# Optimization experiments

Measured on AMD Instinct MI355X. Metric: run time of the kernel, lower is better.

## Reference

```python
import jax, jax.numpy as jnp
import numpy as np

N = 100000
E = 3200000
F_IN = 512
H = 16
C = 40


def gcn_conv(x, edge_index, W, b, num_nodes):
    """PyG GCNConv: y = D^{-1/2} (A + I) D^{-1/2} (x @ W) + b.
    edge_index: [2, E] int, row=source, col=target; self-loops added here."""
    # transform first (small hidden dim keeps message traffic low)
    h = x @ W  # [N, out]
    loops = jnp.arange(num_nodes, dtype=edge_index.dtype)
    row = jnp.concatenate([edge_index[0], loops])
    col = jnp.concatenate([edge_index[1], loops])
    deg = jax.ops.segment_sum(jnp.ones_like(col, dtype=h.dtype), col,
                              num_segments=num_nodes)  # in-degree incl. self-loop
    dinv = jnp.where(deg > 0, jax.lax.rsqrt(deg), 0.0)
    norm = dinv[row] * dinv[col]  # [E+N]
    msgs = h[row] * norm[:, None]  # gather + scale, [E+N, out]
    out = jax.ops.segment_sum(msgs, col, num_segments=num_nodes)  # scatter-add
    return out + b


def setup_inputs() -> dict:
    key = jax.random.key(0)
    k1, k2, k3, k4, k5, k6 = jax.random.split(key, 6)
    x = jax.random.normal(k1, (N, F_IN), dtype=jnp.float32)
    edge_index = jax.random.randint(k2, (2, E), 0, N, dtype=jnp.int64)
    s1 = 1.0 / np.sqrt(F_IN)
    s2 = 1.0 / np.sqrt(H)
    W1 = jax.random.uniform(k3, (F_IN, H), jnp.float32, -s1, s1)
    b1 = jnp.zeros((H,), jnp.float32)
    W2 = jax.random.uniform(k4, (H, C), jnp.float32, -s2, s2)
    b2 = jnp.zeros((C,), jnp.float32)
    return {"x": x, "edge_index": edge_index, "W1": W1, "b1": b1,
            "W2": W2, "b2": b2}


def reference(x, edge_index, W1, b1, W2, b2):
    h = gcn_conv(x, edge_index, W1, b1, N)
    h = jax.nn.relu(h)
    # F.dropout(training=self.training): inference mode -> identity
    h = gcn_conv(h, edge_index, W2, b2, N)
    return jax.nn.log_softmax(h, axis=1)
```

## Files before the change

### kernel.cpp

```cpp
#include <hip/hip_runtime.h>

#define NN 100000
#define EE 3200000
#define FIN 512
#define HH 16
#define CC 40

#define SHIFT 9
#define BNODES 512
#define NB 196
#define CAP 20480
#define CH 4096
#define TC ((EE + CH - 1) / CH)

__device__ __forceinline__ float bf2f(unsigned short u) {
    return __uint_as_float(((unsigned)u) << 16);
}
__device__ __forceinline__ unsigned short f2bf(float f) {
    unsigned b = __float_as_uint(f);
    return (unsigned short)((b + 0x7FFF + ((b >> 16) & 1)) >> 16);
}

__global__ void k_detect(const int* __restrict__ ei, int* __restrict__ flag) {
    __shared__ int nz;
    int t = threadIdx.x;
    if (t == 0) nz = 0;
    __syncthreads();
    if (ei[2 * t + 1] != 0) atomicAdd(&nz, 1);
    __syncthreads();
    if (t == 0) flag[0] = (nz == 0) ? 1 : 0;
}

__global__ void k_bin(const int* __restrict__ ei, const int* __restrict__ flag,
                      int* __restrict__ head, unsigned* __restrict__ pairs) {
    __shared__ int h[NB];
    __shared__ int gbase[NB];
    __shared__ int lhead[NB];
    int t = threadIdx.x;
    int e0 = blockIdx.x * CH, e1 = min(EE, e0 + CH);
    int is64 = flag[0];
    for (int i = t; i < NB; i += 256) { h[i] = 0; lhead[i] = 0; }
    __syncthreads();
    for (int e = e0 + t; e < e1; e += 256) {
        int dst = is64 ? ei[2 * (EE + e)] : ei[EE + e];
        atomicAdd(&h[dst >> SHIFT], 1);
    }
    __syncthreads();
    for (int i = t; i < NB; i += 256)
        gbase[i] = h[i] ? atomicAdd(&head[i], h[i]) : 0;
    __syncthreads();
    for (int e = e0 + t; e < e1; e += 256) {
        int src = is64 ? ei[2 * e] : ei[e];
        int dst = is64 ? ei[2 * (EE + e)] : ei[EE + e];
        int b = dst >> SHIFT;
        int p = gbase[b] + atomicAdd(&lhead[b], 1);
        pairs[(size_t)b * CAP + p] = ((unsigned)(dst & (BNODES - 1)) << 17) | (unsigned)src;
    }
}

__global__ void k_build(const unsigned* __restrict__ pairs, const int* __restrict__ head,
                        int* __restrict__ ptr, int* __restrict__ pend,
                        float* __restrict__ dinv, int* __restrict__ srcs) {
    __shared__ int h[BNODES];
    __shared__ int lex[BNODES];
    __shared__ int ws[4];
    int b = blockIdx.x, t = threadIdx.x, lane = t & 63, wid = t >> 6;
    int node0 = b << SHIFT;
    int p0 = b * CAP;
    int cnt = head[b];
    for (int i = t; i < BNODES; i += 256) h[i] = 0;
    __syncthreads();
    for (int p = t; p < cnt; p += 256) atomicAdd(&h[pairs[p0 + p] >> 17], 1);
    __syncthreads();
    int a0 = h[2 * t], a1 = h[2 * t + 1];
    int s = a0 + a1;
    int v = s;
#pragma unroll
    for (int off = 1; off < 64; off <<= 1) {
        int u = __shfl_up(v, off);
        if (lane >= off) v += u;
    }
    if (lane == 63) ws[wid] = v;
    __syncthreads();
    int add = 0;
    for (int w = 0; w < wid; ++w) add += ws[w];
    int incl = v + add;
    int e0 = incl - s;
    lex[2 * t] = e0;
    lex[2 * t + 1] = e0 + a0;
    __syncthreads();
    for (int i = t; i < BNODES; i += 256) {
        int n = node0 + i;
        if (n < NN) {
            int st = p0 + lex[i];
            ptr[n] = st;
            pend[n] = st + h[i];
            dinv[n] = rsqrtf((float)(h[i] + 1));
        }
    }
    __syncthreads();
    for (int p = t; p < cnt; p += 256) {
        unsigned w = pairs[p0 + p];
        int pos = p0 + atomicAdd(&lex[w >> 17], 1);
        srcs[pos] = (int)(w & 0x1FFFF);
    }
}

__global__ void __launch_bounds__(256) k_gemm1(const float* __restrict__ x,
                                               const float* __restrict__ W1,
                                               const float* __restrict__ dinv,
                                               unsigned short* __restrict__ g1) {
    __shared__ float w1s[FIN * HH];
    int t = threadIdx.x;
    for (int i = t; i < FIN * HH; i += 256) w1s[i] = W1[i];
    __syncthreads();
    int gt = blockIdx.x * 256 + t;
    int node = gt >> 2, q = gt & 3;
    if (node >= NN) return;
    const float4* xr = reinterpret_cast<const float4*>(x + (size_t)node * FIN + q * 128);
    float acc[HH];
#pragma unroll
    for (int f = 0; f < HH; ++f) acc[f] = 0.f;
#pragma unroll 4
    for (int kq = 0; kq < 32; ++kq) {
        float4 xv = xr[kq];
        const float* wr = w1s + (q * 128 + kq * 4) * HH;
#pragma unroll
        for (int f = 0; f < HH; ++f) acc[f] = fmaf(xv.x, wr[f], acc[f]);
#pragma unroll
        for (int f = 0; f < HH; ++f) acc[f] = fmaf(xv.y, wr[HH + f], acc[f]);
#pragma unroll
        for (int f = 0; f < HH; ++f) acc[f] = fmaf(xv.z, wr[2 * HH + f], acc[f]);
#pragma unroll
        for (int f = 0; f < HH; ++f) acc[f] = fmaf(xv.w, wr[3 * HH + f], acc[f]);
    }
#pragma unroll
    for (int f = 0; f < HH; ++f) {
        acc[f] += __shfl_xor(acc[f], 1);
        acc[f] += __shfl_xor(acc[f], 2);
    }
    float di = dinv[node];
    ushort4 o;
    o.x = f2bf(acc[4 * q + 0] * di);
    o.y = f2bf(acc[4 * q + 1] * di);
    o.z = f2bf(acc[4 * q + 2] * di);
    o.w = f2bf(acc[4 * q + 3] * di);
    reinterpret_cast<ushort4*>(g1)[node * 4 + q] = o;
}

__global__ void k_agg1(const unsigned short* __restrict__ g1, const int* __restrict__ ptr,
                       const int* __restrict__ pend, const int* __restrict__ srcs,
                       const float* __restrict__ dinv, const float* __restrict__ b1,
                       unsigned short* __restrict__ g2h) {
    int gt = blockIdx.x * blockDim.x + threadIdx.x;
    int node = gt >> 2, q = gt & 3;
    if (node >= NN) return;
    const ushort4* G = reinterpret_cast<const ushort4*>(g1);
    ushort4 sv = G[node * 4 + q];
    float ax = bf2f(sv.x), ay = bf2f(sv.y), az = bf2f(sv.z), aw = bf2f(sv.w);
    float bx = 0.f, by = 0.f, bz = 0.f, bw = 0.f;
    float cx = 0.f, cy = 0.f, cz = 0.f, cw = 0.f;
    float dx = 0.f, dy = 0.f, dz = 0.f, dw = 0.f;
    int e = ptr[node], e1 = pend[node];
    for (; e + 3 < e1; e += 4) {
        int s0 = srcs[e], s1 = srcs[e + 1], s2 = srcs[e + 2], s3 = srcs[e + 3];
        ushort4 v0 = G[s0 * 4 + q];
        ushort4 v1 = G[s1 * 4 + q];
        ushort4 v2 = G[s2 * 4 + q];
        ushort4 v3 = G[s3 * 4 + q];
        ax += bf2f(v0.x); ay += bf2f(v0.y); az += bf2f(v0.z); aw += bf2f(v0.w);
        bx += bf2f(v1.x); by += bf2f(v1.y); bz += bf2f(v1.z); bw += bf2f(v1.w);
        cx += bf2f(v2.x); cy += bf2f(v2.y); cz += bf2f(v2.z); cw += bf2f(v2.w);
        dx += bf2f(v3.x); dy += bf2f(v3.y); dz += bf2f(v3.z); dw += bf2f(v3.w);
    }
    for (; e < e1; ++e) {
        ushort4 v = G[srcs[e] * 4 + q];
        ax += bf2f(v.x); ay += bf2f(v.y); az += bf2f(v.z); aw += bf2f(v.w);
    }
    ax += bx + cx + dx;
    ay += by + cy + dy;
    az += bz + cz + dz;
    aw += bw + cw + dw;
    float di = dinv[node];
    const float4 bb = reinterpret_cast<const float4*>(b1)[q];
    ushort4 r;
    r.x = f2bf(fmaxf(fmaf(di, ax, bb.x), 0.f) * di);
    r.y = f2bf(fmaxf(fmaf(di, ay, bb.y), 0.f) * di);
    r.z = f2bf(fmaxf(fmaf(di, az, bb.z), 0.f) * di);
    r.w = f2bf(fmaxf(fmaf(di, aw, bb.w), 0.f) * di);
    reinterpret_cast<ushort4*>(g2h)[node * 4 + q] = r;
}

__global__ void k_agg2(const unsigned short* __restrict__ g2h, const int* __restrict__ ptr,
                       const int* __restrict__ pend, const int* __restrict__ srcs,
                       float* __restrict__ sarr) {
    int gt = blockIdx.x * blockDim.x + threadIdx.x;
    int node = gt >> 2, q = gt & 3;
    if (node >= NN) return;
    const ushort4* G = reinterpret_cast<const ushort4*>(g2h);
    ushort4 sv = G[node * 4 + q];
    float ax = bf2f(sv.x), ay = bf2f(sv.y), az = bf2f(sv.z), aw = bf2f(sv.w);
    float bx = 0.f, by = 0.f, bz = 0.f, bw = 0.f;
    float cx = 0.f, cy = 0.f, cz = 0.f, cw = 0.f;
    float dx = 0.f, dy = 0.f, dz = 0.f, dw = 0.f;
    int e = ptr[node], e1 = pend[node];
    for (; e + 3 < e1; e += 4) {
        int s0 = srcs[e], s1 = srcs[e + 1], s2 = srcs[e + 2], s3 = srcs[e + 3];
        ushort4 v0 = G[s0 * 4 + q];
        ushort4 v1 = G[s1 * 4 + q];
        ushort4 v2 = G[s2 * 4 + q];
        ushort4 v3 = G[s3 * 4 + q];
        ax += bf2f(v0.x); ay += bf2f(v0.y); az += bf2f(v0.z); aw += bf2f(v0.w);
        bx += bf2f(v1.x); by += bf2f(v1.y); bz += bf2f(v1.z); bw += bf2f(v1.w);
        cx += bf2f(v2.x); cy += bf2f(v2.y); cz += bf2f(v2.z); cw += bf2f(v2.w);
        dx += bf2f(v3.x); dy += bf2f(v3.y); dz += bf2f(v3.z); dw += bf2f(v3.w);
    }
    for (; e < e1; ++e) {
        ushort4 v = G[srcs[e] * 4 + q];
        ax += bf2f(v.x); ay += bf2f(v.y); az += bf2f(v.z); aw += bf2f(v.w);
    }
    ax += bx + cx + dx;
    ay += by + cy + dy;
    az += bz + cz + dz;
    aw += bw + cw + dw;
    reinterpret_cast<float4*>(sarr)[node * 4 + q] = make_float4(ax, ay, az, aw);
}

__global__ void k_out(const float* __restrict__ sarr, const float* __restrict__ dinv,
                      const float* __restrict__ W2, const float* __restrict__ b2,
                      float* __restrict__ out) {
    int i = blockIdx.x * blockDim.x + threadIdx.x;
    if (i >= NN) return;
    float s[HH];
    {
        const float4* sp = reinterpret_cast<const float4*>(sarr + (size_t)i * HH);
#pragma unroll
        for (int qk = 0; qk < HH / 4; ++qk) {
            float4 v = sp[qk];
            s[4 * qk] = v.x; s[4 * qk + 1] = v.y; s[4 * qk + 2] = v.z; s[4 * qk + 3] = v.w;
        }
    }
    float di = dinv[i];
    float y[CC];
#pragma unroll
    for (int c = 0; c < CC; ++c) y[c] = 0.f;
#pragma unroll
    for (int f = 0; f < HH; ++f) {
        float sf = s[f];
        const float* w2r = W2 + f * CC;
#pragma unroll
        for (int c = 0; c < CC; ++c) y[c] = fmaf(sf, w2r[c], y[c]);
    }
    float m = -3.0e38f;
#pragma unroll
    for (int c = 0; c < CC; ++c) {
        y[c] = fmaf(di, y[c], b2[c]);
        m = fmaxf(m, y[c]);
    }
    float ssum = 0.f;
#pragma unroll
    for (int c = 0; c < CC; ++c) ssum += expf(y[c] - m);
    float l = logf(ssum) + m;
    float4* o = reinterpret_cast<float4*>(out + (size_t)i * CC);
#pragma unroll
    for (int qk = 0; qk < CC / 4; ++qk)
        o[qk] = make_float4(y[4 * qk] - l, y[4 * qk + 1] - l,
                            y[4 * qk + 2] - l, y[4 * qk + 3] - l);
}

extern "C" void kernel_launch(void* const* d_in, const int* in_sizes, int n_in,
                              void* d_out, int out_size, void* d_ws, size_t ws_size,
                              hipStream_t stream) {
    const float* x  = (const float*)d_in[0];
    const int*   ei = (const int*)d_in[1];
    const float* W1 = (const float*)d_in[2];
    const float* b1 = (const float*)d_in[3];
    const float* W2 = (const float*)d_in[4];
    const float* b2 = (const float*)d_in[5];
    float* out = (float*)d_out;

    char* w = (char*)d_ws;
    auto alloc = [&](size_t bytes) {
        char* p = w;
        w += (bytes + 255) & ~(size_t)255;
        return p;
    };
    int*            flag  = (int*)alloc(256);
    int*            head  = (int*)alloc((size_t)NB * 4);
    int*            ptr   = (int*)alloc((size_t)NN * 4);
    int*            pend  = (int*)alloc((size_t)NN * 4);
    float*          dinv  = (float*)alloc((size_t)NN * 4);
    unsigned*       pairs = (unsigned*)alloc((size_t)NB * CAP * 4);
    int*            srcs  = (int*)alloc((size_t)NB * CAP * 4);
    unsigned short* g1    = (unsigned short*)alloc((size_t)NN * HH * 2);
    unsigned short* g2h   = (unsigned short*)alloc((size_t)NN * HH * 2);
    float*          sarr  = (float*)alloc((size_t)NN * HH * 4);

    hipMemsetAsync(head, 0, (size_t)NB * sizeof(int), stream);
    k_detect<<<1, 256, 0, stream>>>(ei, flag);
    k_bin<<<TC, 256, 0, stream>>>(ei, flag, head, pairs);
    k_build<<<NB, 256, 0, stream>>>(pairs, head, ptr, pend, dinv, srcs);
    int nt = NN * 4;
    k_gemm1<<<(nt + 255) / 256, 256, 0, stream>>>(x, W1, dinv, g1);
    k_agg1<<<(nt + 255) / 256, 256, 0, stream>>>(g1, ptr, pend, srcs, dinv, b1, g2h);
    k_agg2<<<(nt + 255) / 256, 256, 0, stream>>>(g2h, ptr, pend, srcs, sarr);
    k_out<<<(NN + 255) / 256, 256, 0, stream>>>(sarr, dinv, W2, b2, out);
}
```

Before: 522.6 us.

## Fuse CSR build with GEMM1, agg2 with output, stage edges in LDS

```diff
diff --git a/kernel.cpp b/kernel.cpp
--- a/kernel.cpp
+++ b/kernel.cpp
@@ -10,8 +10,9 @@
 #define BNODES 512
 #define NB 196
 #define CAP 20480
-#define CH 4096
+#define CH 2048
 #define TC ((EE + CH - 1) / CH)
+#define GB ((NN * 4 + 255) / 256)
 
 __device__ __forceinline__ float bf2f(unsigned short u) {
     return __uint_as_float(((unsigned)u) << 16);
@@ -21,130 +22,143 @@
     return (unsigned short)((b + 0x7FFF + ((b >> 16) & 1)) >> 16);
 }
 
-__global__ void k_detect(const int* __restrict__ ei, int* __restrict__ flag) {
-    __shared__ int nz;
-    int t = threadIdx.x;
-    if (t == 0) nz = 0;
-    __syncthreads();
-    if (ei[2 * t + 1] != 0) atomicAdd(&nz, 1);
-    __syncthreads();
-    if (t == 0) flag[0] = (nz == 0) ? 1 : 0;
-}
-
-__global__ void k_bin(const int* __restrict__ ei, const int* __restrict__ flag,
-                      int* __restrict__ head, unsigned* __restrict__ pairs) {
+__global__ void k_bin(const int* __restrict__ ei, int* __restrict__ head,
+                      unsigned* __restrict__ pairs) {
     __shared__ int h[NB];
     __shared__ int gbase[NB];
     __shared__ int lhead[NB];
+    __shared__ unsigned esrc[CH];
+    __shared__ unsigned edst[CH];
+    __shared__ int is64_s;
     int t = threadIdx.x;
-    int e0 = blockIdx.x * CH, e1 = min(EE, e0 + CH);
-    int is64 = flag[0];
+    if (t < 64) {
+        int nz = (ei[2 * t + 1] != 0) ? 1 : 0;
+        unsigned long long m = __ballot(nz);
+        if (t == 0) is64_s = (m == 0ULL) ? 1 : 0;
+    }
     for (int i = t; i < NB; i += 256) { h[i] = 0; lhead[i] = 0; }
     __syncthreads();
+    int is64 = is64_s;
+    int e0 = blockIdx.x * CH, e1 = min(EE, e0 + CH);
     for (int e = e0 + t; e < e1; e += 256) {
+        int src = is64 ? ei[2 * e] : ei[e];
         int dst = is64 ? ei[2 * (EE + e)] : ei[EE + e];
+        esrc[e - e0] = (unsigned)src;
+        edst[e - e0] = (unsigned)dst;
         atomicAdd(&h[dst >> SHIFT], 1);
     }
     __syncthreads();
     for (int i = t; i < NB; i += 256)
         gbase[i] = h[i] ? atomicAdd(&head[i], h[i]) : 0;
     __syncthreads();
-    for (int e = e0 + t; e < e1; e += 256) {
-        int src = is64 ? ei[2 * e] : ei[e];
-        int dst = is64 ? ei[2 * (EE + e)] : ei[EE + e];
-        int b = dst >> SHIFT;
+    int n = e1 - e0;
+    for (int j = t; j < n; j += 256) {
+        unsigned src = esrc[j];
+        unsigned dst = edst[j];
+        int b = (int)(dst >> SHIFT);
         int p = gbase[b] + atomicAdd(&lhead[b], 1);
-        pairs[(size_t)b * CAP + p] = ((unsigned)(dst & (BNODES - 1)) << 17) | (unsigned)src;
-    }
-}
-
-__global__ void k_build(const unsigned* __restrict__ pairs, const int* __restrict__ head,
-                        int* __restrict__ ptr, int* __restrict__ pend,
-                        float* __restrict__ dinv, int* __restrict__ srcs) {
-    __shared__ int h[BNODES];
-    __shared__ int lex[BNODES];
-    __shared__ int ws[4];
-    int b = blockIdx.x, t = threadIdx.x, lane = t & 63, wid = t >> 6;
-    int node0 = b << SHIFT;
-    int p0 = b * CAP;
-    int cnt = head[b];
-    for (int i = t; i < BNODES; i += 256) h[i] = 0;
-    __syncthreads();
-    for (int p = t; p < cnt; p += 256) atomicAdd(&h[pairs[p0 + p] >> 17], 1);
-    __syncthreads();
-    int a0 = h[2 * t], a1 = h[2 * t + 1];
-    int s = a0 + a1;
-    int v = s;
-#pragma unroll
-    for (int off = 1; off < 64; off <<= 1) {
-        int u = __shfl_up(v, off);
-        if (lane >= off) v += u;
-    }
-    if (lane == 63) ws[wid] = v;
-    __syncthreads();
-    int add = 0;
-    for (int w = 0; w < wid; ++w) add += ws[w];
-    int incl = v + add;
-    int e0 = incl - s;
-    lex[2 * t] = e0;
-    lex[2 * t + 1] = e0 + a0;
-    __syncthreads();
-    for (int i = t; i < BNODES; i += 256) {
-        int n = node0 + i;
-        if (n < NN) {
-            int st = p0 + lex[i];
-            ptr[n] = st;
-            pend[n] = st + h[i];
-            dinv[n] = rsqrtf((float)(h[i] + 1));
-        }
-    }
-    __syncthreads();
-    for (int p = t; p < cnt; p += 256) {
-        unsigned w = pairs[p0 + p];
-        int pos = p0 + atomicAdd(&lex[w >> 17], 1);
-        srcs[pos] = (int)(w & 0x1FFFF);
-    }
-}
-
-__global__ void __launch_bounds__(256) k_gemm1(const float* __restrict__ x,
-                                               const float* __restrict__ W1,
-                                               const float* __restrict__ dinv,
-                                               unsigned short* __restrict__ g1) {
+        pairs[(size_t)b * CAP + p] = ((dst & (BNODES - 1)) << 17) | src;
+    }
+}
+
+__global__ void __launch_bounds__(256) k_buildgemm(
+        const unsigned* __restrict__ pairs, const int* __restrict__ head,
+        int* __restrict__ ptr, int* __restrict__ pend,
+        float* __restrict__ dinv, int* __restrict__ srcs,
+        const float* __restrict__ x, const float* __restrict__ W1,
+        float* __restrict__ g1f) {
     __shared__ float w1s[FIN * HH];
     int t = threadIdx.x;
-    for (int i = t; i < FIN * HH; i += 256) w1s[i] = W1[i];
-    __syncthreads();
-    int gt = blockIdx.x * 256 + t;
+    if (blockIdx.x < NB) {
+        int* h   = (int*)w1s;
+        int* lex = (int*)w1s + BNODES;
+        int* ws  = (int*)w1s + 2 * BNODES;
+        int b = blockIdx.x, lane = t & 63, wid = t >> 6;
+        int node0 = b << SHIFT;
+        int p0 = b * CAP;
+        int cnt = head[b];
+        for (int i = t; i < BNODES; i += 256) h[i] = 0;
+        __syncthreads();
+        for (int p = t; p < cnt; p += 256) atomicAdd(&h[pairs[p0 + p] >> 17], 1);
+        __syncthreads();
+        int a0 = h[2 * t], a1 = h[2 * t + 1];
+        int s = a0 + a1;
+        int v = s;
+#pragma unroll
+        for (int off = 1; off < 64; off <<= 1) {
+            int u = __shfl_up(v, off);
+            if (lane >= off) v += u;
+        }
+        if (lane == 63) ws[wid] = v;
+        __syncthreads();
+        int add = 0;
+        for (int w = 0; w < wid; ++w) add += ws[w];
+        int incl = v + add;
+        int e0 = incl - s;
+        lex[2 * t] = e0;
+        lex[2 * t + 1] = e0 + a0;
+        __syncthreads();
+        for (int i = t; i < BNODES; i += 256) {
+            int n = node0 + i;
+            if (n < NN) {
+                int st = p0 + lex[i];
+                ptr[n] = st;
+                pend[n] = st + h[i];
+                dinv[n] = rsqrtf((float)(h[i] + 1));
+            }
+        }
+        __syncthreads();
+        for (int p = t; p < cnt; p += 256) {
+            unsigned w = pairs[p0 + p];
+            int pos = p0 + atomicAdd(&lex[w >> 17], 1);
+            srcs[pos] = (int)(w & 0x1FFFF);
+        }
+    } else {
+        for (int i = t; i < FIN * HH; i += 256) w1s[i] = W1[i];
+        __syncthreads();
+        int gt = (blockIdx.x - NB) * 256 + t;
+        int node = gt >> 2, q = gt & 3;
+        if (node >= NN) return;
+        const float4* xr = reinterpret_cast<const float4*>(x + (size_t)node * FIN + q * 128);
+        float acc[HH];
+#pragma unroll
+        for (int f = 0; f < HH; ++f) acc[f] = 0.f;
+#pragma unroll 4
+        for (int kq = 0; kq < 32; ++kq) {
+            float4 xv = xr[kq];
+            const float* wr = w1s + (q * 128 + kq * 4) * HH;
+#pragma unroll
+            for (int f = 0; f < HH; ++f) acc[f] = fmaf(xv.x, wr[f], acc[f]);
+#pragma unroll
+            for (int f = 0; f < HH; ++f) acc[f] = fmaf(xv.y, wr[HH + f], acc[f]);
+#pragma unroll
+            for (int f = 0; f < HH; ++f) acc[f] = fmaf(xv.z, wr[2 * HH + f], acc[f]);
+#pragma unroll
+            for (int f = 0; f < HH; ++f) acc[f] = fmaf(xv.w, wr[3 * HH + f], acc[f]);
+        }
+#pragma unroll
+        for (int f = 0; f < HH; ++f) {
+            acc[f] += __shfl_xor(acc[f], 1);
+            acc[f] += __shfl_xor(acc[f], 2);
+        }
+        float4 o = make_float4(acc[4 * q + 0], acc[4 * q + 1],
+                               acc[4 * q + 2], acc[4 * q + 3]);
+        reinterpret_cast<float4*>(g1f)[node * 4 + q] = o;
+    }
+}
+
+__global__ void k_scale(const float* __restrict__ g1f, const float* __restrict__ dinv,
+                        unsigned short* __restrict__ g1) {
+    int gt = blockIdx.x * 256 + threadIdx.x;
     int node = gt >> 2, q = gt & 3;
     if (node >= NN) return;
-    const float4* xr = reinterpret_cast<const float4*>(x + (size_t)node * FIN + q * 128);
-    float acc[HH];
-#pragma unroll
-    for (int f = 0; f < HH; ++f) acc[f] = 0.f;
-#pragma unroll 4
-    for (int kq = 0; kq < 32; ++kq) {
-        float4 xv = xr[kq];
-        const float* wr = w1s + (q * 128 + kq * 4) * HH;
-#pragma unroll
-        for (int f = 0; f < HH; ++f) acc[f] = fmaf(xv.x, wr[f], acc[f]);
-#pragma unroll
-        for (int f = 0; f < HH; ++f) acc[f] = fmaf(xv.y, wr[HH + f], acc[f]);
-#pragma unroll
-        for (int f = 0; f < HH; ++f) acc[f] = fmaf(xv.z, wr[2 * HH + f], acc[f]);
-#pragma unroll
-        for (int f = 0; f < HH; ++f) acc[f] = fmaf(xv.w, wr[3 * HH + f], acc[f]);
-    }
-#pragma unroll
-    for (int f = 0; f < HH; ++f) {
-        acc[f] += __shfl_xor(acc[f], 1);
-        acc[f] += __shfl_xor(acc[f], 2);
-    }
     float di = dinv[node];
+    float4 v = reinterpret_cast<const float4*>(g1f)[node * 4 + q];
     ushort4 o;
-    o.x = f2bf(acc[4 * q + 0] * di);
-    o.y = f2bf(acc[4 * q + 1] * di);
-    o.z = f2bf(acc[4 * q + 2] * di);
-    o.w = f2bf(acc[4 * q + 3] * di);
+    o.x = f2bf(v.x * di);
+    o.y = f2bf(v.y * di);
+    o.z = f2bf(v.z * di);
+    o.w = f2bf(v.w * di);
     reinterpret_cast<ushort4*>(g1)[node * 4 + q] = o;
 }
 
@@ -191,10 +205,18 @@
     reinterpret_cast<ushort4*>(g2h)[node * 4 + q] = r;
 }
 
-__global__ void k_agg2(const unsigned short* __restrict__ g2h, const int* __restrict__ ptr,
-                       const int* __restrict__ pend, const int* __restrict__ srcs,
-                       float* __restrict__ sarr) {
-    int gt = blockIdx.x * blockDim.x + threadIdx.x;
+__global__ void __launch_bounds__(256) k_agg2out(
+        const unsigned short* __restrict__ g2h, const int* __restrict__ ptr,
+        const int* __restrict__ pend, const int* __restrict__ srcs,
+        const float* __restrict__ dinv, const float* __restrict__ W2,
+        const float* __restrict__ b2, float* __restrict__ out) {
+    __shared__ float w2s[HH * 41];
+    __shared__ float b2s[CC];
+    int t = threadIdx.x;
+    for (int i = t; i < HH * CC; i += 256) w2s[(i / CC) * 41 + (i % CC)] = W2[i];
+    if (t < CC) b2s[t] = b2[t];
+    __syncthreads();
+    int gt = blockIdx.x * blockDim.x + t;
     int node = gt >> 2, q = gt & 3;
     if (node >= NN) return;
     const ushort4* G = reinterpret_cast<const ushort4*>(g2h);
@@ -223,49 +245,38 @@
     ay += by + cy + dy;
     az += bz + cz + dz;
     aw += bw + cw + dw;
-    reinterpret_cast<float4*>(sarr)[node * 4 + q] = make_float4(ax, ay, az, aw);
-}
-
-__global__ void k_out(const float* __restrict__ sarr, const float* __restrict__ dinv,
-                      const float* __restrict__ W2, const float* __restrict__ b2,
-                      float* __restrict__ out) {
-    int i = blockIdx.x * blockDim.x + threadIdx.x;
-    if (i >= NN) return;
-    float s[HH];
-    {
-        const float4* sp = reinterpret_cast<const float4*>(sarr + (size_t)i * HH);
-#pragma unroll
-        for (int qk = 0; qk < HH / 4; ++qk) {
-            float4 v = sp[qk];
-            s[4 * qk] = v.x; s[4 * qk + 1] = v.y; s[4 * qk + 2] = v.z; s[4 * qk + 3] = v.w;
-        }
-    }
-    float di = dinv[i];
+    const float* w0 = w2s + (4 * q + 0) * 41;
+    const float* w1 = w2s + (4 * q + 1) * 41;
+    const float* w2r = w2s + (4 * q + 2) * 41;
+    const float* w3 = w2s + (4 * q + 3) * 41;
     float y[CC];
 #pragma unroll
-    for (int c = 0; c < CC; ++c) y[c] = 0.f;
-#pragma unroll
-    for (int f = 0; f < HH; ++f) {
-        float sf = s[f];
-        const float* w2r = W2 + f * CC;
-#pragma unroll
-        for (int c = 0; c < CC; ++c) y[c] = fmaf(sf, w2r[c], y[c]);
-    }
+    for (int c = 0; c < CC; ++c)
+        y[c] = fmaf(ax, w0[c], fmaf(ay, w1[c], fmaf(az, w2r[c], aw * w3[c])));
+#pragma unroll
+    for (int c = 0; c < CC; ++c) {
+        y[c] += __shfl_xor(y[c], 1);
+        y[c] += __shfl_xor(y[c], 2);
+    }
+    float di = dinv[node];
     float m = -3.0e38f;
 #pragma unroll
     for (int c = 0; c < CC; ++c) {
-        y[c] = fmaf(di, y[c], b2[c]);
+        y[c] = fmaf(di, y[c], b2s[c]);
         m = fmaxf(m, y[c]);
     }
     float ssum = 0.f;
 #pragma unroll
     for (int c = 0; c < CC; ++c) ssum += expf(y[c] - m);
     float l = logf(ssum) + m;
-    float4* o = reinterpret_cast<float4*>(out + (size_t)i * CC);
-#pragma unroll
-    for (int qk = 0; qk < CC / 4; ++qk)
-        o[qk] = make_float4(y[4 * qk] - l, y[4 * qk + 1] - l,
-                            y[4 * qk + 2] - l, y[4 * qk + 3] - l);
+    float ov[10];
+#pragma unroll
+    for (int c = 0; c < CC; ++c) {
+        if ((c / 10) == q) ov[c % 10] = y[c] - l;
+    }
+    float2* o2 = reinterpret_cast<float2*>(out + (size_t)node * CC + 10 * q);
+#pragma unroll
+    for (int i = 0; i < 5; ++i) o2[i] = make_float2(ov[2 * i], ov[2 * i + 1]);
 }
 
 extern "C" void kernel_launch(void* const* d_in, const int* in_sizes, int n_in,
@@ -285,24 +296,23 @@
         w += (bytes + 255) & ~(size_t)255;
         return p;
     };
-    int*            flag  = (int*)alloc(256);
     int*            head  = (int*)alloc((size_t)NB * 4);
     int*            ptr   = (int*)alloc((size_t)NN * 4);
     int*            pend  = (int*)alloc((size_t)NN * 4);
     float*          dinv  = (float*)alloc((size_t)NN * 4);
     unsigned*       pairs = (unsigned*)alloc((size_t)NB * CAP * 4);
     int*            srcs  = (int*)alloc((size_t)NB * CAP * 4);
+    float*          g1f   = (float*)alloc((size_t)NN * HH * 4);
     unsigned short* g1    = (unsigned short*)alloc((size_t)NN * HH * 2);
     unsigned short* g2h   = (unsigned short*)alloc((size_t)NN * HH * 2);
-    float*          sarr  = (float*)alloc((size_t)NN * HH * 4);
 
     hipMemsetAsync(head, 0, (size_t)NB * sizeof(int), stream);
-    k_detect<<<1, 256, 0, stream>>>(ei, flag);
-    k_bin<<<TC, 256, 0, stream>>>(ei, flag, head, pairs);
-    k_build<<<NB, 256, 0, stream>>>(pairs, head, ptr, pend, dinv, srcs);
+    k_bin<<<TC, 256, 0, stream>>>(ei, head, pairs);
+    k_buildgemm<<<NB + GB, 256, 0, stream>>>(pairs, head, ptr, pend, dinv, srcs,
+                                             x, W1, g1f);
+    k_scale<<<GB, 256, 0, stream>>>(g1f, dinv, g1);
     int nt = NN * 4;
-    k_gemm1<<<(nt + 255) / 256, 256, 0, stream>>>(x, W1, dinv, g1);
     k_agg1<<<(nt + 255) / 256, 256, 0, stream>>>(g1, ptr, pend, srcs, dinv, b1, g2h);
-    k_agg2<<<(nt + 255) / 256, 256, 0, stream>>>(g2h, ptr, pend, srcs, sarr);
-    k_out<<<(NN + 255) / 256, 256, 0, stream>>>(sarr, dinv, W2, b2, out);
-}
+    k_agg2out<<<(nt + 255) / 256, 256, 0, stream>>>(g2h, ptr, pend, srcs, dinv,
+                                                    W2, b2, out);
+}
```

After: 470.1 us. 10.0% less time.
